# Kernel optimization log

Hardware: AMD Instinct MI355X
Metric: run time of the kernel (lower is better)

Reference implementation:

```python
import jax, jax.numpy as jnp
import numpy as np

NX, NY = 384, 384
H = 1e-4
DT = 5e-9
NT = 192
STRIDE = 4
RHO = 1610.0
F0 = 2.0e6
T0 = 4e-7
AMP = 1e10
GAUSS_A = 5e6

C11_INIT, C22_INIT, C12_INIT = 1.3074e11, 1.15e10, 1.049e10
C16_INIT, C26_INIT, C66_INIT = 3.067e10, 3.75e9, 1.477e10
B11 = (5e10, 2.5e11); B22 = (5e9, 5e10); B12 = (5e9, 5e10)
B16 = (0.0, 6e10); B26 = (0.0, 2e10); B66 = (5e9, 3e10)


def setup_inputs() -> dict:
    # log-parameter fields, constant-initialized as in the module __init__
    full = lambda v: jnp.full((1, NX, NY), np.log(v), dtype=jnp.float32)
    log_C11 = full(C11_INIT)
    log_C22 = full(C22_INIT)
    log_C12 = full(C12_INIT)
    log_C16 = full(abs(C16_INIT) + 1e6)
    log_C26 = full(abs(C26_INIT) + 1e6)
    log_C66 = full(C66_INIT)
    # Gaussian point-load distribution centered at domain center
    Lx, Ly = H * (NX - 1), H * (NY - 1)
    x = np.linspace(-Lx / 2, Lx / 2, NX)
    y = np.linspace(-Ly / 2, Ly / 2, NY)
    X, Y = np.meshgrid(x, y, indexing='ij')
    gauss = (GAUSS_A / np.pi) * np.exp(-GAUSS_A * (X ** 2 + Y ** 2))
    # Ricker wavelet source signal over nt steps
    t = np.arange(NT) * DT
    tau = t - T0
    pft2 = (np.pi * F0 * tau) ** 2
    sig = AMP * (1.0 - 2.0 * pft2) * np.exp(-pft2)
    return {
        'log_C11': log_C11, 'log_C12': log_C12, 'log_C16': log_C16,
        'log_C22': log_C22, 'log_C26': log_C26, 'log_C66': log_C66,
        'gaussian_dist': jnp.asarray(gauss, dtype=jnp.float32),
        'source_signal': jnp.asarray(sig, dtype=jnp.float32),
    }


def _stencils(u, hinv2):
    # u: (B, nx, ny). Zero padding == fixed (u=0) boundary, matching conv2d_fixed.
    up = jnp.pad(u, ((0, 0), (1, 1), (1, 1)))
    d2x = (up[:, :-2, 1:-1] - 2.0 * u + up[:, 2:, 1:-1]) * hinv2
    d2y = (up[:, 1:-1, :-2] - 2.0 * u + up[:, 1:-1, 2:]) * hinv2
    dxy = 0.25 * (up[:, :-2, :-2] - up[:, :-2, 2:] - up[:, 2:, :-2] + up[:, 2:, 2:]) * hinv2
    return d2x, d2y, dxy


def _simulate(log_C11, log_C12, log_C16, log_C22, log_C26, log_C66,
              gaussian_dist, source_signal):
    clip = lambda lc, b: jnp.clip(jnp.exp(lc), b[0], b[1])
    C11 = clip(log_C11, B11); C22 = clip(log_C22, B22); C12 = clip(log_C12, B12)
    C16 = clip(log_C16, B16); C26 = clip(log_C26, B26); C66 = clip(log_C66, B66)
    hinv2 = jnp.float32(1.0 / (H * H))
    dt2 = jnp.float32(DT * DT)
    g = gaussian_dist[None]  # (1, nx, ny)
    C12p66 = C12 + C66

    def step(carry, sig_t):
        ux1, uy1, ux2, uy2 = carry
        dxx_x, dyy_x, dxy_x = _stencils(ux1, hinv2)
        dxx_y, dyy_y, dxy_y = _stencils(uy1, hinv2)
        Lux = (C11 * dxx_x + C66 * dyy_x + C12p66 * dxy_y
               + 2.0 * C16 * dxy_x + C16 * dxx_y + C26 * dyy_y)
        Luy = (C66 * dxx_y + C22 * dyy_y + C12p66 * dxy_x
               + C16 * dxx_x + C26 * dyy_x + 2.0 * C26 * dxy_y)
        # Ricker point source on the y-component (source_component='y')
        ax = Lux / RHO
        ay = (Luy + sig_t * g) / RHO
        ux_new = 2.0 * ux1 - ux2 + dt2 * ax
        uy_new = 2.0 * uy1 - uy2 + dt2 * ay
        return (ux_new, uy_new, ux1, uy1), (ux_new, uy_new)

    z = jnp.zeros((1, NX, NY), dtype=jnp.float32)
    _, (ux_all, uy_all) = jax.lax.scan(step, (z, z, z, z), source_signal)
    # subsample by primary_time_stride -> (1, nt//stride, nx, ny)
    ux_f = jnp.transpose(ux_all[STRIDE - 1::STRIDE], (1, 0, 2, 3))
    uy_f = jnp.transpose(uy_all[STRIDE - 1::STRIDE], (1, 0, 2, 3))
    return jnp.stack([ux_f, uy_f])  # (2, 1, nt_out, nx, ny)


def reference(log_C11, log_C12, log_C16, log_C22, log_C26, log_C66,
              gaussian_dist, source_signal):
    return _simulate(log_C11, log_C12, log_C16, log_C22, log_C26, log_C66,
                     gaussian_dist, source_signal)
```

## Files before the change

kernel.cpp:

```cpp
#include <hip/hip_runtime.h>


typedef float v2f __attribute__((ext_vector_type(2)));

#define NXg 384
#define NYg 384
#define NPT (NXg * NYg)
#define NFRAMES 48

#define OWN 24
#define HALO 12
#define TS 48
#define KSTEPS 12
#define NLAUNCH 16

#define H_   1e-4
#define DT_  5e-9
#define RHO_ 1610.0

#define B11_LO 5e10f
#define B11_HI 2.5e11f
#define B22_LO 5e9f
#define B22_HI 5e10f
#define B12_LO 5e9f
#define B12_HI 5e10f
#define B16_LO 0.0f
#define B16_HI 6e10f
#define B26_LO 0.0f
#define B26_HI 2e10f
#define B66_LO 5e9f
#define B66_HI 3e10f

#define ROW_SHR1 0x111
#define ROW_SHL1 0x101

static __device__ __constant__ float kScale  = (float)(DT_ * DT_ / (H_ * H_) / RHO_);
static __device__ __constant__ float kSrcScl = (float)(DT_ * DT_ / RHO_);

__device__ __forceinline__ float clipf(float v, float lo, float hi) {
    return fminf(fmaxf(v, lo), hi);
}
__device__ __forceinline__ v2f vfma(v2f a, v2f b, v2f c) {
    return __builtin_elementwise_fma(a, b, c);
}
__device__ __forceinline__ v2f vbc(float s) { v2f r; r[0] = s; r[1] = s; return r; }
__device__ __forceinline__ v2f vswap(v2f a) { return __builtin_shufflevector(a, a, 1, 0); }

template <int CTRL>
__device__ __forceinline__ v2f dpp_shift(v2f oldv, v2f src) {
    union { v2f v; int i[2]; } o, s, r;
    o.v = oldv; s.v = src;
    r.i[0] = __builtin_amdgcn_update_dpp(o.i[0], s.i[0], CTRL, 0xf, 0xf, false);
    r.i[1] = __builtin_amdgcn_update_dpp(o.i[1], s.i[1], CTRL, 0xf, 0xf, false);
    return r.v;
}

#define LDS_BARRIER() asm volatile("s_waitcnt lgkmcnt(0)\n\ts_barrier" ::: "memory")


__global__ __launch_bounds__(256)
void setup_kernel(const float* __restrict__ lc11, const float* __restrict__ lc12,
                  const float* __restrict__ lc16, const float* __restrict__ lc22,
                  const float* __restrict__ lc26, const float* __restrict__ lc66,
                  const float* __restrict__ gauss, float* __restrict__ ws) {
    int i = blockIdx.x * blockDim.x + threadIdx.x;
    if (i >= NPT) return;
    float C11 = clipf(expf(lc11[i]), B11_LO, B11_HI);
    float C12 = clipf(expf(lc12[i]), B12_LO, B12_HI);
    float C16 = clipf(expf(lc16[i]), B16_LO, B16_HI);
    float C22 = clipf(expf(lc22[i]), B22_LO, B22_HI);
    float C26 = clipf(expf(lc26[i]), B26_LO, B26_HI);
    float C66 = clipf(expf(lc66[i]), B66_LO, B66_HI);
    float s = kScale;
    float4* C0 = (float4*)ws;
    float4* C1 = (float4*)(ws + 4 * (size_t)NPT);
    C0[i] = make_float4(C11 * s, C22 * s, (C12 + C66) * s, C16 * s);
    C1[i] = make_float4(C26 * s, C66 * s, gauss[i] * kSrcScl, 0.0f);
    float4* s0 = (float4*)(ws + 8 * (size_t)NPT);
    s0[i] = make_float4(0.0f, 0.0f, 0.0f, 0.0f);
}

__global__ __launch_bounds__(256, 1)
void fused_kernel(const float* __restrict__ ws, const float* __restrict__ sig,
                  const float4* __restrict__ inS, float4* __restrict__ outS,
                  float* __restrict__ out, int L) {
    __shared__ v2f sb[2][TS][TS + 1];

    const int tid = threadIdx.x;
    const int tx = tid >> 4;
    const int ty = tid & 15;
    const int r0 = 3 * tx;
    const int c0 = 3 * ty;
    const int gx0 = blockIdx.y * OWN - HALO;
    const int gy0 = blockIdx.x * OWN - HALO;

    const float4* __restrict__ C0 = (const float4*)ws;
    const float4* __restrict__ C1 = (const float4*)(ws + 4 * (size_t)NPT);

    v2f cur[9], old_[9];
    v2f ca[9], cb[9];
    float a12p66[9], a16[9], a26[9], gs[9];
    int gidx[9];

#pragma unroll
    for (int i = 0; i < 3; ++i) {
#pragma unroll
        for (int j = 0; j < 3; ++j) {
            int p = i * 3 + j;
            int gx = gx0 + r0 + i;
            int gy = gy0 + c0 + j;
            bool d = (unsigned)gx < (unsigned)NXg && (unsigned)gy < (unsigned)NYg;
            int g = d ? gx * NYg + gy : 0;
            gidx[p] = g;
            float4 st = d ? inS[g] : make_float4(0, 0, 0, 0);
            v2f c; c[0] = st.x; c[1] = st.y;
            v2f o; o[0] = st.z; o[1] = st.w;
            cur[p] = c; old_[p] = o;
            float4 k0 = d ? C0[g] : make_float4(0, 0, 0, 0);
            float4 k1 = d ? C1[g] : make_float4(0, 0, 0, 0);
            v2f t; t[0] = k0.x; t[1] = k1.y; ca[p] = t;
            v2f u; u[0] = k1.y; u[1] = k0.y; cb[p] = u;
            a12p66[p] = k0.z; a16[p] = k0.w; a26[p] = k1.x; gs[p] = k1.z;
        }
    }

    const int t0 = L * KSTEPS;
    float sigv[KSTEPS];
#pragma unroll
    for (int k = 0; k < KSTEPS; ++k) sigv[k] = sig[t0 + k];

    const int rm = (r0 > 0) ? r0 - 1 : 0;
    const int rp = (r0 + 3 < TS) ? r0 + 3 : TS - 1;
    const int cm = (c0 > 0) ? c0 - 1 : 0;
    const int cp = (c0 + 3 < TS) ? c0 + 3 : TS - 1;

    const bool owned = (tx >= 4) && (tx < 12) && (ty >= 4) && (ty < 12);

#pragma unroll
    for (int j = 0; j < 3; ++j) {
        sb[0][r0 + 0][c0 + j] = cur[0 * 3 + j];
        sb[0][r0 + 2][c0 + j] = cur[2 * 3 + j];
    }
    LDS_BARRIER();

    v2f c20; c20[0] = 2.0f; c20[1] = 0.0f;
    v2f c02; c02[0] = 0.0f; c02[1] = 2.0f;
    const v2f m2 = vbc(-2.0f);
    const v2f qt = vbc(0.25f);
    const v2f two = vbc(2.0f);

#pragma unroll
    for (int s = 1; s <= KSTEPS; ++s) {
        const v2f (*rb)[TS + 1] = sb[(s - 1) & 1];
        v2f (*wb)[TS + 1] = sb[s & 1];
        v2f vsig; vsig[0] = 0.0f; vsig[1] = sigv[s - 1];

        v2f v[5][5];
#pragma unroll
        for (int i = 0; i < 3; ++i)
#pragma unroll
            for (int j = 0; j < 3; ++j)
                v[i + 1][j + 1] = cur[i * 3 + j];
#pragma unroll
        for (int i = 0; i < 3; ++i) {
            v[i + 1][0] = dpp_shift<ROW_SHR1>(cur[i * 3 + 0], cur[i * 3 + 2]);
            v[i + 1][4] = dpp_shift<ROW_SHL1>(cur[i * 3 + 2], cur[i * 3 + 0]);
        }
        v[0][0] = rb[rm][cm];  v[0][4] = rb[rm][cp];
        v[4][0] = rb[rp][cm];  v[4][4] = rb[rp][cp];
#pragma unroll
        for (int j = 0; j < 3; ++j) {
            v[0][j + 1] = rb[rm][c0 + j];
            v[4][j + 1] = rb[rp][c0 + j];
        }

        v2f dh[5][3];
#pragma unroll
        for (int i = 0; i < 5; ++i)
#pragma unroll
            for (int j = 0; j < 3; ++j)
                dh[i][j] = v[i][j + 2] - v[i][j];

#pragma unroll
        for (int i = 0; i < 3; ++i)
#pragma unroll
            for (int j = 0; j < 3; ++j) {
                int p = i * 3 + j;
                v2f c = v[i + 1][j + 1];
                v2f sxx = vfma(m2, c, v[i][j + 1] + v[i + 2][j + 1]);
                v2f syy = vfma(m2, c, v[i + 1][j] + v[i + 1][j + 2]);
                v2f sxy = qt * (dh[i + 2][j] - dh[i][j]);

                v2f t4 = vfma(c20, vbc(sxy[0]), vswap(sxx));
                v2f t5 = vfma(c02, vbc(sxy[1]), vswap(syy));
                v2f Lv = ca[p] * sxx;
                Lv = vfma(cb[p], syy, Lv);
                Lv = vfma(vbc(a12p66[p]), vswap(sxy), Lv);
                Lv = vfma(vbc(a16[p]), t4, Lv);
                Lv = vfma(vbc(a26[p]), t5, Lv);
                Lv = vfma(vsig, vbc(gs[p]), Lv);
                v2f n = vfma(two, c, Lv) - old_[p];
                old_[p] = c;
                cur[p] = n;
            }

        if ((s & 3) == 0 && owned) {
            int f = 3 * L + (s >> 2) - 1;
            float* oux = out + (size_t)f * NPT;
            float* ouy = out + (size_t)(NFRAMES + f) * NPT;
#pragma unroll
            for (int p = 0; p < 9; ++p) {
                oux[gidx[p]] = cur[p][0];
                ouy[gidx[p]] = cur[p][1];
            }
        }

        if (s < KSTEPS) {
#pragma unroll
            for (int j = 0; j < 3; ++j) {
                wb[r0 + 0][c0 + j] = cur[0 * 3 + j];
                wb[r0 + 2][c0 + j] = cur[2 * 3 + j];
            }
            LDS_BARRIER();
        }
    }

    if (owned) {
#pragma unroll
        for (int p = 0; p < 9; ++p) {
            float4 st = make_float4(cur[p][0], cur[p][1], old_[p][0], old_[p][1]);
            outS[gidx[p]] = st;
        }
    }
}

extern "C" void kernel_launch(void* const* d_in, const int* in_sizes, int n_in,
                              void* d_out, int out_size, void* d_ws, size_t ws_size,
                              hipStream_t stream) {
    const float* lc11  = (const float*)d_in[0];
    const float* lc12  = (const float*)d_in[1];
    const float* lc16  = (const float*)d_in[2];
    const float* lc22  = (const float*)d_in[3];
    const float* lc26  = (const float*)d_in[4];
    const float* lc66  = (const float*)d_in[5];
    const float* gauss = (const float*)d_in[6];
    const float* sig   = (const float*)d_in[7];

    float* ws  = (float*)d_ws;
    float* out = (float*)d_out;

    setup_kernel<<<(NPT + 255) / 256, 256, 0, stream>>>(lc11, lc12, lc16, lc22,
                                                        lc26, lc66, gauss, ws);

    float4* set0 = (float4*)(ws + 8 * (size_t)NPT);
    float4* set1 = (float4*)(ws + 12 * (size_t)NPT);

    dim3 grid(NXg / OWN, NYg / OWN);
    for (int L = 0; L < NLAUNCH; ++L) {
        float4* iS = (L & 1) ? set1 : set0;
        float4* oS = (L & 1) ? set0 : set1;
        fused_kernel<<<grid, 256, 0, stream>>>(ws, sig, iS, oS, out, L);
    }
}
```

Measured before the change: 319.0 us.

## Use 768 threads per block with 1x3 points per thread instead of 3x3

Each block now runs 768 threads, and each thread owns a single row of three points instead of a 3x3 patch, so the 48x48 tile is covered by three times as many threads. Row neighbours above and below are read from LDS every step and then shifted with DPP to get the corners. This raises thread-level parallelism and latency hiding and cuts per-thread register pressure. The cost is more LDS reads per point, since rows above and below are no longer reused within a thread, and more waves that must meet at each barrier.

```diff
diff --git a/kernel.cpp b/kernel.cpp
--- a/kernel.cpp
+++ b/kernel.cpp
@@ -13,6 +13,8 @@
 #define TS 48
 #define KSTEPS 12
 #define NLAUNCH 16
+#define NTH 768
+#define TROW 16
 
 #define H_   1e-4
 #define DT_  5e-9
@@ -80,7 +82,7 @@
     s0[i] = make_float4(0.0f, 0.0f, 0.0f, 0.0f);
 }
 
-__global__ __launch_bounds__(256, 1)
+__global__ __launch_bounds__(NTH)
 void fused_kernel(const float* __restrict__ ws, const float* __restrict__ sig,
                   const float4* __restrict__ inS, float4* __restrict__ outS,
                   float* __restrict__ out, int L) {
@@ -89,7 +91,7 @@
     const int tid = threadIdx.x;
     const int tx = tid >> 4;
     const int ty = tid & 15;
-    const int r0 = 3 * tx;
+    const int r0 = tx;
     const int c0 = 3 * ty;
     const int gx0 = blockIdx.y * OWN - HALO;
     const int gy0 = blockIdx.x * OWN - HALO;
@@ -97,31 +99,27 @@
     const float4* __restrict__ C0 = (const float4*)ws;
     const float4* __restrict__ C1 = (const float4*)(ws + 4 * (size_t)NPT);
 
-    v2f cur[9], old_[9];
-    v2f ca[9], cb[9];
-    float a12p66[9], a16[9], a26[9], gs[9];
-    int gidx[9];
-
-#pragma unroll
-    for (int i = 0; i < 3; ++i) {
-#pragma unroll
-        for (int j = 0; j < 3; ++j) {
-            int p = i * 3 + j;
-            int gx = gx0 + r0 + i;
-            int gy = gy0 + c0 + j;
-            bool d = (unsigned)gx < (unsigned)NXg && (unsigned)gy < (unsigned)NYg;
-            int g = d ? gx * NYg + gy : 0;
-            gidx[p] = g;
-            float4 st = d ? inS[g] : make_float4(0, 0, 0, 0);
-            v2f c; c[0] = st.x; c[1] = st.y;
-            v2f o; o[0] = st.z; o[1] = st.w;
-            cur[p] = c; old_[p] = o;
-            float4 k0 = d ? C0[g] : make_float4(0, 0, 0, 0);
-            float4 k1 = d ? C1[g] : make_float4(0, 0, 0, 0);
-            v2f t; t[0] = k0.x; t[1] = k1.y; ca[p] = t;
-            v2f u; u[0] = k1.y; u[1] = k0.y; cb[p] = u;
-            a12p66[p] = k0.z; a16[p] = k0.w; a26[p] = k1.x; gs[p] = k1.z;
-        }
+    v2f cur[3], old_[3];
+    v2f ca[3], cb[3];
+    float a12p66[3], a16[3], a26[3], gs[3];
+    int gidx[3];
+
+#pragma unroll
+    for (int j = 0; j < 3; ++j) {
+        int gx = gx0 + r0;
+        int gy = gy0 + c0 + j;
+        bool d = (unsigned)gx < (unsigned)NXg && (unsigned)gy < (unsigned)NYg;
+        int g = d ? gx * NYg + gy : 0;
+        gidx[j] = g;
+        float4 st = d ? inS[g] : make_float4(0, 0, 0, 0);
+        v2f c; c[0] = st.x; c[1] = st.y;
+        v2f o; o[0] = st.z; o[1] = st.w;
+        cur[j] = c; old_[j] = o;
+        float4 k0 = d ? C0[g] : make_float4(0, 0, 0, 0);
+        float4 k1 = d ? C1[g] : make_float4(0, 0, 0, 0);
+        v2f t; t[0] = k0.x; t[1] = k1.y; ca[j] = t;
+        v2f u; u[0] = k1.y; u[1] = k0.y; cb[j] = u;
+        a12p66[j] = k0.z; a16[j] = k0.w; a26[j] = k1.x; gs[j] = k1.z;
     }
 
     const int t0 = L * KSTEPS;
@@ -130,17 +128,13 @@
     for (int k = 0; k < KSTEPS; ++k) sigv[k] = sig[t0 + k];
 
     const int rm = (r0 > 0) ? r0 - 1 : 0;
-    const int rp = (r0 + 3 < TS) ? r0 + 3 : TS - 1;
-    const int cm = (c0 > 0) ? c0 - 1 : 0;
-    const int cp = (c0 + 3 < TS) ? c0 + 3 : TS - 1;
-
-    const bool owned = (tx >= 4) && (tx < 12) && (ty >= 4) && (ty < 12);
-
-#pragma unroll
-    for (int j = 0; j < 3; ++j) {
-        sb[0][r0 + 0][c0 + j] = cur[0 * 3 + j];
-        sb[0][r0 + 2][c0 + j] = cur[2 * 3 + j];
-    }
+    const int rp = (r0 + 1 < TS) ? r0 + 1 : TS - 1;
+
+    const bool owned = (tx >= 12) && (tx < 36) && (ty >= 4) && (ty < 12);
+
+#pragma unroll
+    for (int j = 0; j < 3; ++j)
+        sb[0][r0][c0 + j] = cur[j];
     LDS_BARRIER();
 
     v2f c20; c20[0] = 2.0f; c20[1] = 0.0f;
@@ -155,81 +149,74 @@
         v2f (*wb)[TS + 1] = sb[s & 1];
         v2f vsig; vsig[0] = 0.0f; vsig[1] = sigv[s - 1];
 
-        v2f v[5][5];
-#pragma unroll
-        for (int i = 0; i < 3; ++i)
-#pragma unroll
-            for (int j = 0; j < 3; ++j)
-                v[i + 1][j + 1] = cur[i * 3 + j];
-#pragma unroll
-        for (int i = 0; i < 3; ++i) {
-            v[i + 1][0] = dpp_shift<ROW_SHR1>(cur[i * 3 + 0], cur[i * 3 + 2]);
-            v[i + 1][4] = dpp_shift<ROW_SHL1>(cur[i * 3 + 2], cur[i * 3 + 0]);
-        }
-        v[0][0] = rb[rm][cm];  v[0][4] = rb[rm][cp];
-        v[4][0] = rb[rp][cm];  v[4][4] = rb[rp][cp];
+        v2f vm[5], vc[5], vp[5];
+        vc[1] = cur[0]; vc[2] = cur[1]; vc[3] = cur[2];
+        vc[0] = dpp_shift<ROW_SHR1>(cur[0], cur[2]);
+        vc[4] = dpp_shift<ROW_SHL1>(cur[2], cur[0]);
+        {
+            v2f a0 = rb[rm][c0], a1 = rb[rm][c0 + 1], a2 = rb[rm][c0 + 2];
+            vm[1] = a0; vm[2] = a1; vm[3] = a2;
+            vm[0] = dpp_shift<ROW_SHR1>(a0, a2);
+            vm[4] = dpp_shift<ROW_SHL1>(a2, a0);
+        }
+        {
+            v2f b0 = rb[rp][c0], b1 = rb[rp][c0 + 1], b2 = rb[rp][c0 + 2];
+            vp[1] = b0; vp[2] = b1; vp[3] = b2;
+            vp[0] = dpp_shift<ROW_SHR1>(b0, b2);
+            vp[4] = dpp_shift<ROW_SHL1>(b2, b0);
+        }
+
+        v2f dhm[3], dhp[3];
 #pragma unroll
         for (int j = 0; j < 3; ++j) {
-            v[0][j + 1] = rb[rm][c0 + j];
-            v[4][j + 1] = rb[rp][c0 + j];
-        }
-
-        v2f dh[5][3];
-#pragma unroll
-        for (int i = 0; i < 5; ++i)
-#pragma unroll
-            for (int j = 0; j < 3; ++j)
-                dh[i][j] = v[i][j + 2] - v[i][j];
-
-#pragma unroll
-        for (int i = 0; i < 3; ++i)
-#pragma unroll
-            for (int j = 0; j < 3; ++j) {
-                int p = i * 3 + j;
-                v2f c = v[i + 1][j + 1];
-                v2f sxx = vfma(m2, c, v[i][j + 1] + v[i + 2][j + 1]);
-                v2f syy = vfma(m2, c, v[i + 1][j] + v[i + 1][j + 2]);
-                v2f sxy = qt * (dh[i + 2][j] - dh[i][j]);
-
-                v2f t4 = vfma(c20, vbc(sxy[0]), vswap(sxx));
-                v2f t5 = vfma(c02, vbc(sxy[1]), vswap(syy));
-                v2f Lv = ca[p] * sxx;
-                Lv = vfma(cb[p], syy, Lv);
-                Lv = vfma(vbc(a12p66[p]), vswap(sxy), Lv);
-                Lv = vfma(vbc(a16[p]), t4, Lv);
-                Lv = vfma(vbc(a26[p]), t5, Lv);
-                Lv = vfma(vsig, vbc(gs[p]), Lv);
-                v2f n = vfma(two, c, Lv) - old_[p];
-                old_[p] = c;
-                cur[p] = n;
-            }
+            dhm[j] = vm[j + 2] - vm[j];
+            dhp[j] = vp[j + 2] - vp[j];
+        }
+
+#pragma unroll
+        for (int j = 0; j < 3; ++j) {
+            v2f c = vc[j + 1];
+            v2f sxx = vfma(m2, c, vm[j + 1] + vp[j + 1]);
+            v2f syy = vfma(m2, c, vc[j] + vc[j + 2]);
+            v2f sxy = qt * (dhp[j] - dhm[j]);
+
+            v2f t4 = vfma(c20, vbc(sxy[0]), vswap(sxx));
+            v2f t5 = vfma(c02, vbc(sxy[1]), vswap(syy));
+            v2f Lv = ca[j] * sxx;
+            Lv = vfma(cb[j], syy, Lv);
+            Lv = vfma(vbc(a12p66[j]), vswap(sxy), Lv);
+            Lv = vfma(vbc(a16[j]), t4, Lv);
+            Lv = vfma(vbc(a26[j]), t5, Lv);
+            Lv = vfma(vsig, vbc(gs[j]), Lv);
+            v2f n = vfma(two, c, Lv) - old_[j];
+            old_[j] = c;
+            cur[j] = n;
+        }
 
         if ((s & 3) == 0 && owned) {
             int f = 3 * L + (s >> 2) - 1;
             float* oux = out + (size_t)f * NPT;
             float* ouy = out + (size_t)(NFRAMES + f) * NPT;
 #pragma unroll
-            for (int p = 0; p < 9; ++p) {
-                oux[gidx[p]] = cur[p][0];
-                ouy[gidx[p]] = cur[p][1];
+            for (int j = 0; j < 3; ++j) {
+                oux[gidx[j]] = cur[j][0];
+                ouy[gidx[j]] = cur[j][1];
             }
         }
 
         if (s < KSTEPS) {
 #pragma unroll
-            for (int j = 0; j < 3; ++j) {
-                wb[r0 + 0][c0 + j] = cur[0 * 3 + j];
-                wb[r0 + 2][c0 + j] = cur[2 * 3 + j];
-            }
+            for (int j = 0; j < 3; ++j)
+                wb[r0][c0 + j] = cur[j];
             LDS_BARRIER();
         }
     }
 
     if (owned) {
 #pragma unroll
-        for (int p = 0; p < 9; ++p) {
-            float4 st = make_float4(cur[p][0], cur[p][1], old_[p][0], old_[p][1]);
-            outS[gidx[p]] = st;
+        for (int j = 0; j < 3; ++j) {
+            float4 st = make_float4(cur[j][0], cur[j][1], old_[j][0], old_[j][1]);
+            outS[gidx[j]] = st;
         }
     }
 }
@@ -259,6 +246,6 @@
     for (int L = 0; L < NLAUNCH; ++L) {
         float4* iS = (L & 1) ? set1 : set0;
         float4* oS = (L & 1) ? set0 : set1;
-        fused_kernel<<<grid, 256, 0, stream>>>(ws, sig, iS, oS, out, L);
-    }
-}
+        fused_kernel<<<grid, NTH, 0, stream>>>(ws, sig, iS, oS, out, L);
+    }
+}
```

New measurement: 294.4 us, median of 2. 1.08x faster.
